# Performance work log

Hardware: AMD Instinct MI355X
Metric: run time of the kernel (lower is better)

The kernel has to match this reference:

```python
import jax, jax.numpy as jnp
import numpy as np

B, S, D, H, DFF = 4, 2048, 1024, 16, 4096
HD = D // H
EPS = 1e-12

def _layernorm(x, g, b):
    mu = jnp.mean(x, axis=-1, keepdims=True)
    var = jnp.mean(jnp.square(x - mu), axis=-1, keepdims=True)
    return (x - mu) * jax.lax.rsqrt(var + EPS) * g + b

def setup_inputs() -> dict:
    key = jax.random.key(0)
    ks = jax.random.split(key, 12)
    sd = 0.02
    inp = {
        'hidden_states': jax.random.normal(ks[0], (B, S, D), jnp.float32),
        'attention_mask': jnp.zeros((B, 1, 1, S), jnp.float32),
        'Wq': jax.random.normal(ks[1], (D, D), jnp.float32) * sd,
        'bq': jnp.zeros((D,), jnp.float32),
        'Wk': jax.random.normal(ks[2], (D, D), jnp.float32) * sd,
        'bk': jnp.zeros((D,), jnp.float32),
        'Wv': jax.random.normal(ks[3], (D, D), jnp.float32) * sd,
        'bv': jnp.zeros((D,), jnp.float32),
        'Wo': jax.random.normal(ks[4], (D, D), jnp.float32) * sd,
        'bo': jnp.zeros((D,), jnp.float32),
        'ln1_g': jnp.ones((D,), jnp.float32),
        'ln1_b': jnp.zeros((D,), jnp.float32),
        'Wi': jax.random.normal(ks[5], (D, DFF), jnp.float32) * sd,
        'bi': jnp.zeros((DFF,), jnp.float32),
        'Wo2': jax.random.normal(ks[6], (DFF, D), jnp.float32) * sd,
        'bo2': jnp.zeros((D,), jnp.float32),
        'ln2_g': jnp.ones((D,), jnp.float32),
        'ln2_b': jnp.zeros((D,), jnp.float32),
    }
    return inp

def reference(hidden_states, attention_mask, Wq, bq, Wk, bk, Wv, bv, Wo, bo,
              ln1_g, ln1_b, Wi, bi, Wo2, bo2, ln2_g, ln2_b):
    x = hidden_states  # [B,S,D]
    # project and split heads -> [B,H,S,hd]
    def heads(t):
        return t.reshape(B, S, H, HD).transpose(0, 2, 1, 3)
    q = heads(x @ Wq + bq)
    k = heads(x @ Wk + bk)
    v = heads(x @ Wv + bv)
    scores = jnp.einsum('bhqd,bhkd->bhqk', q, k) / np.float32(np.sqrt(HD))
    scores = scores + attention_mask  # additive mask broadcast [B,1,1,S]
    weights = jax.nn.softmax(scores, axis=-1)
    ctx = jnp.einsum('bhqk,bhkd->bhqd', weights, v)
    ctx = ctx.transpose(0, 2, 1, 3).reshape(B, S, D)
    attn_out = _layernorm(ctx @ Wo + bo + x, ln1_g, ln1_b)
    # FFN (gelu) with residual + LayerNorm
    h = jax.nn.gelu(attn_out @ Wi + bi, approximate=False)
    out = _layernorm(h @ Wo2 + bo2 + attn_out, ln2_g, ln2_b)
    return out
```

## Files before the change

### kernel.cpp

```cpp
#include <hip/hip_runtime.h>
#include <hip/hip_bf16.h>
#include <math.h>

#define B_   4
#define S_   2048
#define D_   1024
#define H_   16
#define HD_  64
#define DFF_ 4096
#define M_   (B_*S_)

typedef __bf16 bf16x8 __attribute__((ext_vector_type(8)));
typedef __bf16 bf16x4 __attribute__((ext_vector_type(4)));
typedef float  floatx4 __attribute__((ext_vector_type(4)));

__device__ __forceinline__ float  b2f(__bf16 v) { return (float)v; }
__device__ __forceinline__ __bf16 f2b(float v)  { return (__bf16)v; }

__device__ __forceinline__ void async_ld16(const void* g, void* l) {
    __builtin_amdgcn_global_load_lds(
        (const __attribute__((address_space(1))) unsigned int*)g,
        (__attribute__((address_space(3))) unsigned int*)l, 16, 0, 0);
}

__global__ void transpose_conv_kernel(const float* __restrict__ in,
                                      __bf16* __restrict__ out, int R, int C,
                                      float scale)
{
    __shared__ float t[32][33];
    int c0 = blockIdx.x * 32, r0 = blockIdx.y * 32;
    int tx = threadIdx.x, ty = threadIdx.y;
    for (int i = ty; i < 32; i += 8)
        t[i][tx] = in[(long)(r0 + i) * C + c0 + tx];
    __syncthreads();
    for (int i = ty; i < 32; i += 8)
        out[(long)(c0 + i) * R + r0 + tx] = f2b(t[tx][i] * scale);
}

__global__ void vt_transpose_kernel(const __bf16* __restrict__ qkv,
                                    __bf16* __restrict__ vtg)
{
    __shared__ __bf16 t[32][34];
    int b  = blockIdx.z;
    int h  = blockIdx.y >> 1;
    int d0 = (blockIdx.y & 1) * 32;
    int s0 = blockIdx.x * 32;
    int tx = threadIdx.x, ty = threadIdx.y;
    for (int i = ty; i < 32; i += 8)
        t[i][tx] = qkv[(long)(b * S_ + s0 + i) * 3072 + 2048 + h * 64 + d0 + tx];
    __syncthreads();
    for (int i = ty; i < 32; i += 8)
        vtg[((long)(b * H_ + h) * 64 + d0 + i) * S_ + s0 + tx] = t[tx][i];
}

__global__ void f2b_kernel(const float* __restrict__ in, __bf16* __restrict__ out,
                           long n)
{
    long i = ((long)blockIdx.x * 256 + threadIdx.x) * 8;
    if (i >= n) return;
    float4 a = *(const float4*)&in[i];
    float4 c = *(const float4*)&in[i + 4];
    union { __bf16 h[8]; uint4 u; } p;
    p.h[0] = f2b(a.x); p.h[1] = f2b(a.y); p.h[2] = f2b(a.z); p.h[3] = f2b(a.w);
    p.h[4] = f2b(c.x); p.h[5] = f2b(c.y); p.h[6] = f2b(c.z); p.h[7] = f2b(c.w);
    *(uint4*)&out[i] = p.u;
}

__global__ void bias_concat_kernel(const float* __restrict__ bq,
                                   const float* __restrict__ bk,
                                   const float* __restrict__ bv,
                                   float* __restrict__ dst)
{
    int i = blockIdx.x * 256 + threadIdx.x;
    if (i >= 3 * D_) return;
    float v = (i < D_) ? bq[i] * 0.125f
            : (i < 2 * D_) ? bk[i - D_] : bv[i - 2 * D_];
    dst[i] = v;
}

template<int MODE>
__global__ __launch_bounds__(256, 2)
void gemm_kernel(const __bf16* __restrict__ A, const __bf16* __restrict__ Bt,
                 const float* __restrict__ bias, const float* __restrict__ resid,
                 float* __restrict__ Cf, __bf16* __restrict__ Cb,
                 int M, int N, int K)
{
    __shared__ __bf16 sA[128 * 64];
    __shared__ __bf16 sB[128 * 64];

    const int tid  = threadIdx.x;
    const int lane = tid & 63;
    const int wave = tid >> 6;
    const int wm   = (wave >> 1) * 64;
    const int wn   = (wave & 1) * 64;
    const long bm  = (long)blockIdx.y * 128;
    const long bn  = (long)blockIdx.x * 128;

    floatx4 acc[4][4];
#pragma unroll
    for (int i = 0; i < 4; ++i)
#pragma unroll
        for (int j = 0; j < 4; ++j)
#pragma unroll
            for (int r = 0; r < 4; ++r) acc[i][j][r] = 0.0f;

    const int mrow = lane & 15;
    const int quad = lane >> 4;
    const int koff0 = ((0 * 4 + quad) ^ (mrow & 7)) * 8;
    const int koff1 = ((1 * 4 + quad) ^ (mrow & 7)) * 8;

    for (int k0 = 0; k0 < K; k0 += 64) {
        __syncthreads();
#pragma unroll
        for (int t = 0; t < 4; ++t) {
            int ci  = tid + t * 256;
            int row = ci >> 3;
            int col = ((ci & 7) ^ (row & 7)) << 3;
            async_ld16(A  + (bm + row) * (long)K + k0 + col, &sA[ci * 8]);
            async_ld16(Bt + (bn + row) * (long)K + k0 + col, &sB[ci * 8]);
        }
        __syncthreads();

#pragma unroll
        for (int s = 0; s < 2; ++s) {
            const int ko = s ? koff1 : koff0;
            bf16x8 a[4], b[4];
#pragma unroll
            for (int i = 0; i < 4; ++i)
                a[i] = *(const bf16x8*)&sA[(wm + i * 16 + mrow) * 64 + ko];
#pragma unroll
            for (int j = 0; j < 4; ++j)
                b[j] = *(const bf16x8*)&sB[(wn + j * 16 + mrow) * 64 + ko];
#pragma unroll
            for (int i = 0; i < 4; ++i)
#pragma unroll
                for (int j = 0; j < 4; ++j)
                    acc[i][j] = __builtin_amdgcn_mfma_f32_16x16x32_bf16(
                        a[i], b[j], acc[i][j], 0, 0, 0);
        }
    }

    const int rq = quad * 4;
    const int cn = lane & 15;
#pragma unroll
    for (int i = 0; i < 4; ++i) {
#pragma unroll
        for (int j = 0; j < 4; ++j) {
            long col = bn + wn + j * 16 + cn;
            float bv = bias[col];
#pragma unroll
            for (int r = 0; r < 4; ++r) {
                long row = bm + wm + i * 16 + rq + r;
                float v = acc[i][j][r] + bv;
                if (MODE == 0) {
                    Cb[row * N + col] = f2b(v);
                } else if (MODE == 1) {
                    Cf[row * N + col] = v + resid[row * N + col];
                } else {
                    float g = 0.5f * v * (1.0f + erff(v * 0.70710678118654752f));
                    Cb[row * N + col] = f2b(g);
                }
            }
        }
    }
}

__global__ __launch_bounds__(256, 2)
void attn_kernel(const __bf16* __restrict__ QKV, const __bf16* __restrict__ VT,
                 const float* __restrict__ mask, __bf16* __restrict__ ctx)
{
    __shared__ __bf16 Ks[2][64 * 64];
    __shared__ __bf16 Vt[2][64 * 64];
    __shared__ __bf16 Ps[64 * 64];

    const int tid  = threadIdx.x;
    const int lane = tid & 63;
    const int wave = tid >> 6;
    const int w16  = wave * 16;
    const int b    = blockIdx.z, h = blockIdx.y;
    const int q0   = blockIdx.x * 64;
    const int cn   = lane & 15;
    const int quad = lane >> 4;
    const int rq   = quad * 4;
    const int koff0 = ((0 * 4 + quad) ^ (cn & 7)) * 8;
    const int koff1 = ((1 * 4 + quad) ^ (cn & 7)) * 8;

    const long vbase = ((long)(b * H_ + h) * 64) * S_;

    auto STAGE = [&](int bufi, int k0) {
#pragma unroll
        for (int t = 0; t < 2; ++t) {
            int ci = tid + t * 256;
            int r  = ci >> 3;
            int cz = ((ci & 7) ^ (r & 7)) << 3;
            async_ld16(QKV + (long)(b * S_ + k0 + r) * 3072 + 1024 + h * 64 + cz,
                       &Ks[bufi][ci * 8]);
            async_ld16(VT + vbase + (long)r * S_ + k0 + cz, &Vt[bufi][ci * 8]);
        }
    };

#pragma unroll
    for (int t = 0; t < 2; ++t) {
        int ci = tid + t * 256;
        int qr = ci >> 3, dc = ((ci & 7) ^ (qr & 7)) << 3;
        async_ld16(QKV + (long)(b * S_ + q0 + qr) * 3072 + h * 64 + dc,
                   &Ps[ci * 8]);
    }
    STAGE(0, 0);
    asm volatile("s_waitcnt vmcnt(0)" ::: "memory");
    __builtin_amdgcn_s_barrier();
    __builtin_amdgcn_sched_barrier(0);

    const bf16x8 aq0 = *(const bf16x8*)&Ps[(w16 + cn) * 64 + koff0];
    const bf16x8 aq1 = *(const bf16x8*)&Ps[(w16 + cn) * 64 + koff1];

    float l_[4];
    floatx4 o_[4];
#pragma unroll
    for (int r = 0; r < 4; ++r) l_[r] = 0.0f;
#pragma unroll
    for (int jt = 0; jt < 4; ++jt)
#pragma unroll
        for (int r = 0; r < 4; ++r) o_[jt][r] = 0.0f;

    int cur = 0;
    for (int k0 = 0; k0 < S_; k0 += 64) {
        if (k0 + 64 < S_) STAGE(cur ^ 1, k0 + 64);

        floatx4 st[4];
#pragma unroll
        for (int jt = 0; jt < 4; ++jt)
#pragma unroll
            for (int r = 0; r < 4; ++r) st[jt][r] = 0.0f;
#pragma unroll
        for (int jt = 0; jt < 4; ++jt) {
            bf16x8 b0 = *(const bf16x8*)&Ks[cur][(jt * 16 + cn) * 64 + koff0];
            bf16x8 b1 = *(const bf16x8*)&Ks[cur][(jt * 16 + cn) * 64 + koff1];
            st[jt] = __builtin_amdgcn_mfma_f32_16x16x32_bf16(aq0, b0, st[jt], 0, 0, 0);
            st[jt] = __builtin_amdgcn_mfma_f32_16x16x32_bf16(aq1, b1, st[jt], 0, 0, 0);
        }
#pragma unroll
        for (int jt = 0; jt < 4; ++jt) {
            float mv = mask[(long)b * S_ + k0 + jt * 16 + cn] - 8.0f;
#pragma unroll
            for (int r = 0; r < 4; ++r) {
                float p = __expf(st[jt][r] + mv);
                st[jt][r] = p;
                l_[r] += p;
            }
        }
#pragma unroll
        for (int jt = 0; jt < 4; ++jt)
#pragma unroll
            for (int r = 0; r < 4; ++r) {
                int prow = w16 + rq + r;
                int pcol = (((jt * 2 + (cn >> 3)) ^ (prow & 7)) << 3) + (cn & 7);
                Ps[prow * 64 + pcol] = f2b(st[jt][r]);
            }

        {
            bf16x8 ap0 = *(const bf16x8*)&Ps[(w16 + cn) * 64 + koff0];
            bf16x8 ap1 = *(const bf16x8*)&Ps[(w16 + cn) * 64 + koff1];
#pragma unroll
            for (int jt = 0; jt < 4; ++jt) {
                bf16x8 b0 = *(const bf16x8*)&Vt[cur][(jt * 16 + cn) * 64 + koff0];
                bf16x8 b1 = *(const bf16x8*)&Vt[cur][(jt * 16 + cn) * 64 + koff1];
                o_[jt] = __builtin_amdgcn_mfma_f32_16x16x32_bf16(ap0, b0, o_[jt], 0, 0, 0);
                o_[jt] = __builtin_amdgcn_mfma_f32_16x16x32_bf16(ap1, b1, o_[jt], 0, 0, 0);
            }
        }

        asm volatile("s_waitcnt vmcnt(0) lgkmcnt(0)" ::: "memory");
        __builtin_amdgcn_s_barrier();
        __builtin_amdgcn_sched_barrier(0);
        cur ^= 1;
    }

#pragma unroll
    for (int r = 0; r < 4; ++r) {
        float l = l_[r];
        l += __shfl_xor(l, 1);
        l += __shfl_xor(l, 2);
        l += __shfl_xor(l, 4);
        l += __shfl_xor(l, 8);
        float linv = 1.0f / l;
        long rowg = (long)(b * S_ + q0 + w16 + rq + r) * D_ + h * 64;
#pragma unroll
        for (int jt = 0; jt < 4; ++jt)
            ctx[rowg + jt * 16 + cn] = f2b(o_[jt][r] * linv);
    }
}

__global__ __launch_bounds__(256)
void ln_kernel(const float* __restrict__ X, const float* __restrict__ gamma,
               const float* __restrict__ beta, float* __restrict__ out,
               __bf16* __restrict__ outb)
{
    const long row = blockIdx.x;
    const int tid = threadIdx.x;
    const float* x = X + row * D_;
    float4 v = *(const float4*)&x[tid * 4];
    float s  = v.x + v.y + v.z + v.w;
    float s2 = v.x * v.x + v.y * v.y + v.z * v.z + v.w * v.w;
    for (int off = 32; off > 0; off >>= 1) {
        s  += __shfl_down(s, off);
        s2 += __shfl_down(s2, off);
    }
    __shared__ float red[8];
    int wave = tid >> 6, lane = tid & 63;
    if (lane == 0) { red[wave] = s; red[4 + wave] = s2; }
    __syncthreads();
    float ts  = red[0] + red[1] + red[2] + red[3];
    float ts2 = red[4] + red[5] + red[6] + red[7];
    float mu  = ts * (1.0f / D_);
    float var = ts2 * (1.0f / D_) - mu * mu;
    float rs  = rsqrtf(fmaxf(var, 0.0f) + 1e-12f);
    float4 g = *(const float4*)&gamma[tid * 4];
    float4 b = *(const float4*)&beta[tid * 4];
    float4 o;
    o.x = (v.x - mu) * rs * g.x + b.x;
    o.y = (v.y - mu) * rs * g.y + b.y;
    o.z = (v.z - mu) * rs * g.z + b.z;
    o.w = (v.w - mu) * rs * g.w + b.w;
    *(float4*)&out[row * D_ + tid * 4] = o;
    if (outb) {
        bf16x4 ob;
        ob[0] = f2b(o.x); ob[1] = f2b(o.y); ob[2] = f2b(o.z); ob[3] = f2b(o.w);
        *(bf16x4*)&outb[row * D_ + tid * 4] = ob;
    }
}

extern "C" void kernel_launch(void* const* d_in, const int* in_sizes, int n_in,
                              void* d_out, int out_size, void* d_ws, size_t ws_size,
                              hipStream_t stream)
{
    const float* hid  = (const float*)d_in[0];
    const float* mask = (const float*)d_in[1];
    const float* Wq   = (const float*)d_in[2];
    const float* bq   = (const float*)d_in[3];
    const float* Wk   = (const float*)d_in[4];
    const float* bk   = (const float*)d_in[5];
    const float* Wv   = (const float*)d_in[6];
    const float* bv   = (const float*)d_in[7];
    const float* Wo   = (const float*)d_in[8];
    const float* bo   = (const float*)d_in[9];
    const float* g1   = (const float*)d_in[10];
    const float* b1   = (const float*)d_in[11];
    const float* Wi   = (const float*)d_in[12];
    const float* bi   = (const float*)d_in[13];
    const float* Wo2  = (const float*)d_in[14];
    const float* bo2  = (const float*)d_in[15];
    const float* g2   = (const float*)d_in[16];
    const float* b2   = (const float*)d_in[17];
    float* out = (float*)d_out;

    char* w = (char*)d_ws;
    auto take = [&](size_t bytes) { char* p = w; w += bytes; return p; };
    __bf16* wqkvb = (__bf16*)take((size_t)3 * D_ * D_ * 2);
    __bf16* wob   = (__bf16*)take((size_t)D_ * D_ * 2);
    __bf16* wib   = (__bf16*)take((size_t)D_ * DFF_ * 2);
    __bf16* wo2b  = (__bf16*)take((size_t)D_ * DFF_ * 2);
    float*  qkvbias = (float*)take(16384);
    __bf16* qkv   = (__bf16*)take((size_t)M_ * 3 * D_ * 2);
    __bf16* ctxb  = (__bf16*)take((size_t)M_ * D_ * 2);
    __bf16* hb    = (__bf16*)take((size_t)M_ * D_ * 2);
    float*  tmp      = (float*)take((size_t)M_ * D_ * 4);
    float*  attn_out = (float*)take((size_t)M_ * D_ * 4);
    __bf16* hbuf = qkv;
    __bf16* vtg  = hb;
    __bf16* attn_out_b = hb;
    (void)in_sizes; (void)n_in; (void)out_size; (void)ws_size;

    dim3 tb(32, 8);
    transpose_conv_kernel<<<dim3(D_/32, D_/32), tb, 0, stream>>>(Wq, wqkvb,            D_, D_, 0.125f);
    transpose_conv_kernel<<<dim3(D_/32, D_/32), tb, 0, stream>>>(Wk, wqkvb + D_*D_,    D_, D_, 1.0f);
    transpose_conv_kernel<<<dim3(D_/32, D_/32), tb, 0, stream>>>(Wv, wqkvb + 2*D_*D_,  D_, D_, 1.0f);
    transpose_conv_kernel<<<dim3(D_/32, D_/32), tb, 0, stream>>>(Wo, wob, D_, D_, 1.0f);
    transpose_conv_kernel<<<dim3(DFF_/32, D_/32), tb, 0, stream>>>(Wi, wib, D_, DFF_, 1.0f);
    transpose_conv_kernel<<<dim3(D_/32, DFF_/32), tb, 0, stream>>>(Wo2, wo2b, DFF_, D_, 1.0f);
    bias_concat_kernel<<<12, 256, 0, stream>>>(bq, bk, bv, qkvbias);
    f2b_kernel<<<(M_*D_/8 + 255)/256, 256, 0, stream>>>(hid, hb, (long)M_*D_);

    gemm_kernel<0><<<dim3(3*D_/128, M_/128), 256, 0, stream>>>(
        hb, wqkvb, qkvbias, nullptr, nullptr, qkv, M_, 3*D_, D_);

    vt_transpose_kernel<<<dim3(S_/32, H_*2, B_), tb, 0, stream>>>(qkv, vtg);

    attn_kernel<<<dim3(S_/64, H_, B_), 256, 0, stream>>>(qkv, vtg, mask, ctxb);

    gemm_kernel<1><<<dim3(D_/128, M_/128), 256, 0, stream>>>(
        ctxb, wob, bo, hid, tmp, nullptr, M_, D_, D_);
    ln_kernel<<<M_, 256, 0, stream>>>(tmp, g1, b1, attn_out, attn_out_b);

    gemm_kernel<2><<<dim3(DFF_/128, M_/128), 256, 0, stream>>>(
        attn_out_b, wib, bi, nullptr, nullptr, hbuf, M_, DFF_, D_);
    gemm_kernel<1><<<dim3(D_/128, M_/128), 256, 0, stream>>>(
        hbuf, wo2b, bo2, attn_out, tmp, nullptr, M_, D_, DFF_);
    ln_kernel<<<M_, 256, 0, stream>>>(tmp, g2, b2, out, nullptr);
}
```

Before: 569.0 us.

## Fuse prep kernels into one launch, remap attention blocks per XCD, prefetch mask

Merges the six weight transpose-convert launches, the bias concat and the hidden-state bf16 conversion into a single prep kernel dispatched on block index, removing seven launches. The attention grid becomes one-dimensional and is remapped so blocks of the same (batch, head) land on the same XCD, which should improve L2 reuse of K/V. Mask values are now prefetched one tile ahead, and MFMA sections are wrapped in s_setprio to favour matrix issue. The branchy prep kernel adds divergence-free but uneven block work.

```diff
diff --git a/kernel.cpp b/kernel.cpp
--- a/kernel.cpp
+++ b/kernel.cpp
@@ -23,18 +23,51 @@
         (__attribute__((address_space(3))) unsigned int*)l, 16, 0, 0);
 }
 
-__global__ void transpose_conv_kernel(const float* __restrict__ in,
-                                      __bf16* __restrict__ out, int R, int C,
-                                      float scale)
+__global__ __launch_bounds__(256)
+void prep_kernel(const float* __restrict__ Wq, const float* __restrict__ Wk,
+                 const float* __restrict__ Wv, const float* __restrict__ Wo,
+                 const float* __restrict__ Wi, const float* __restrict__ Wo2,
+                 const float* __restrict__ bq, const float* __restrict__ bk,
+                 const float* __restrict__ bv, const float* __restrict__ hid,
+                 __bf16* __restrict__ wqkvb, __bf16* __restrict__ wob,
+                 __bf16* __restrict__ wib, __bf16* __restrict__ wo2b,
+                 float* __restrict__ qkvbias, __bf16* __restrict__ hb)
 {
     __shared__ float t[32][33];
-    int c0 = blockIdx.x * 32, r0 = blockIdx.y * 32;
-    int tx = threadIdx.x, ty = threadIdx.y;
-    for (int i = ty; i < 32; i += 8)
-        t[i][tx] = in[(long)(r0 + i) * C + c0 + tx];
-    __syncthreads();
-    for (int i = ty; i < 32; i += 8)
-        out[(long)(c0 + i) * R + r0 + tx] = f2b(t[tx][i] * scale);
+    const int bid = blockIdx.x;
+    const int tid = threadIdx.x;
+
+    if (bid < 12288) {
+        const float* in; __bf16* outp; int R, C, nx, lid; float scale = 1.0f;
+        if (bid < 1024)      { in = Wq;  outp = wqkvb;           R = D_;   C = D_;   nx = 32;  lid = bid;        scale = 0.125f; }
+        else if (bid < 2048) { in = Wk;  outp = wqkvb + D_*D_;   R = D_;   C = D_;   nx = 32;  lid = bid - 1024; }
+        else if (bid < 3072) { in = Wv;  outp = wqkvb + 2*D_*D_; R = D_;   C = D_;   nx = 32;  lid = bid - 2048; }
+        else if (bid < 4096) { in = Wo;  outp = wob;             R = D_;   C = D_;   nx = 32;  lid = bid - 3072; }
+        else if (bid < 8192) { in = Wi;  outp = wib;             R = D_;   C = DFF_; nx = 128; lid = bid - 4096; }
+        else                 { in = Wo2; outp = wo2b;            R = DFF_; C = D_;   nx = 32;  lid = bid - 8192; }
+        const int c0 = (lid % nx) * 32, r0 = (lid / nx) * 32;
+        const int tx = tid & 31, ty = tid >> 5;
+        for (int i = ty; i < 32; i += 8)
+            t[i][tx] = in[(long)(r0 + i) * C + c0 + tx];
+        __syncthreads();
+        for (int i = ty; i < 32; i += 8)
+            outp[(long)(c0 + i) * R + r0 + tx] = f2b(t[tx][i] * scale);
+    } else if (bid < 16384) {
+        long i = ((long)(bid - 12288) * 256 + tid) * 8;
+        if (i >= (long)M_ * D_) return;
+        float4 a = *(const float4*)&hid[i];
+        float4 c = *(const float4*)&hid[i + 4];
+        union { __bf16 h[8]; uint4 u; } p;
+        p.h[0] = f2b(a.x); p.h[1] = f2b(a.y); p.h[2] = f2b(a.z); p.h[3] = f2b(a.w);
+        p.h[4] = f2b(c.x); p.h[5] = f2b(c.y); p.h[6] = f2b(c.z); p.h[7] = f2b(c.w);
+        *(uint4*)&hb[i] = p.u;
+    } else {
+        int i = (bid - 16384) * 256 + tid;
+        if (i >= 3 * D_) return;
+        float v = (i < D_) ? bq[i] * 0.125f
+                : (i < 2 * D_) ? bk[i - D_] : bv[i - 2 * D_];
+        qkvbias[i] = v;
+    }
 }
 
 __global__ void vt_transpose_kernel(const __bf16* __restrict__ qkv,
@@ -51,31 +84,6 @@
     __syncthreads();
     for (int i = ty; i < 32; i += 8)
         vtg[((long)(b * H_ + h) * 64 + d0 + i) * S_ + s0 + tx] = t[tx][i];
-}
-
-__global__ void f2b_kernel(const float* __restrict__ in, __bf16* __restrict__ out,
-                           long n)
-{
-    long i = ((long)blockIdx.x * 256 + threadIdx.x) * 8;
-    if (i >= n) return;
-    float4 a = *(const float4*)&in[i];
-    float4 c = *(const float4*)&in[i + 4];
-    union { __bf16 h[8]; uint4 u; } p;
-    p.h[0] = f2b(a.x); p.h[1] = f2b(a.y); p.h[2] = f2b(a.z); p.h[3] = f2b(a.w);
-    p.h[4] = f2b(c.x); p.h[5] = f2b(c.y); p.h[6] = f2b(c.z); p.h[7] = f2b(c.w);
-    *(uint4*)&out[i] = p.u;
-}
-
-__global__ void bias_concat_kernel(const float* __restrict__ bq,
-                                   const float* __restrict__ bk,
-                                   const float* __restrict__ bv,
-                                   float* __restrict__ dst)
-{
-    int i = blockIdx.x * 256 + threadIdx.x;
-    if (i >= 3 * D_) return;
-    float v = (i < D_) ? bq[i] * 0.125f
-            : (i < 2 * D_) ? bk[i - D_] : bv[i - 2 * D_];
-    dst[i] = v;
 }
 
 template<int MODE>
@@ -177,8 +185,15 @@
     const int lane = tid & 63;
     const int wave = tid >> 6;
     const int w16  = wave * 16;
-    const int b    = blockIdx.z, h = blockIdx.y;
-    const int q0   = blockIdx.x * 64;
+
+    const int ibk  = blockIdx.x;
+    const int xcd  = ibk & 7;
+    const int tt   = ibk >> 3;
+    const int head_lin = xcd * 8 + (tt >> 5);
+    const int q0   = (tt & 31) * 64;
+    const int b    = head_lin >> 4;
+    const int h    = head_lin & 15;
+
     const int cn   = lane & 15;
     const int quad = lane >> 4;
     const int rq   = quad * 4;
@@ -207,6 +222,10 @@
                    &Ps[ci * 8]);
     }
     STAGE(0, 0);
+    float mv[4];
+#pragma unroll
+    for (int jt = 0; jt < 4; ++jt)
+        mv[jt] = mask[(long)b * S_ + jt * 16 + cn] - 8.0f;
     asm volatile("s_waitcnt vmcnt(0)" ::: "memory");
     __builtin_amdgcn_s_barrier();
     __builtin_amdgcn_sched_barrier(0);
@@ -225,13 +244,20 @@
 
     int cur = 0;
     for (int k0 = 0; k0 < S_; k0 += 64) {
-        if (k0 + 64 < S_) STAGE(cur ^ 1, k0 + 64);
+        float mvn[4];
+        if (k0 + 64 < S_) {
+            STAGE(cur ^ 1, k0 + 64);
+#pragma unroll
+            for (int jt = 0; jt < 4; ++jt)
+                mvn[jt] = mask[(long)b * S_ + k0 + 64 + jt * 16 + cn] - 8.0f;
+        }
 
         floatx4 st[4];
 #pragma unroll
         for (int jt = 0; jt < 4; ++jt)
 #pragma unroll
             for (int r = 0; r < 4; ++r) st[jt][r] = 0.0f;
+        __builtin_amdgcn_s_setprio(1);
 #pragma unroll
         for (int jt = 0; jt < 4; ++jt) {
             bf16x8 b0 = *(const bf16x8*)&Ks[cur][(jt * 16 + cn) * 64 + koff0];
@@ -239,12 +265,12 @@
             st[jt] = __builtin_amdgcn_mfma_f32_16x16x32_bf16(aq0, b0, st[jt], 0, 0, 0);
             st[jt] = __builtin_amdgcn_mfma_f32_16x16x32_bf16(aq1, b1, st[jt], 0, 0, 0);
         }
+        __builtin_amdgcn_s_setprio(0);
 #pragma unroll
         for (int jt = 0; jt < 4; ++jt) {
-            float mv = mask[(long)b * S_ + k0 + jt * 16 + cn] - 8.0f;
 #pragma unroll
             for (int r = 0; r < 4; ++r) {
-                float p = __expf(st[jt][r] + mv);
+                float p = __expf(st[jt][r] + mv[jt]);
                 st[jt][r] = p;
                 l_[r] += p;
             }
@@ -261,6 +287,7 @@
         {
             bf16x8 ap0 = *(const bf16x8*)&Ps[(w16 + cn) * 64 + koff0];
             bf16x8 ap1 = *(const bf16x8*)&Ps[(w16 + cn) * 64 + koff1];
+            __builtin_amdgcn_s_setprio(1);
 #pragma unroll
             for (int jt = 0; jt < 4; ++jt) {
                 bf16x8 b0 = *(const bf16x8*)&Vt[cur][(jt * 16 + cn) * 64 + koff0];
@@ -268,11 +295,16 @@
                 o_[jt] = __builtin_amdgcn_mfma_f32_16x16x32_bf16(ap0, b0, o_[jt], 0, 0, 0);
                 o_[jt] = __builtin_amdgcn_mfma_f32_16x16x32_bf16(ap1, b1, o_[jt], 0, 0, 0);
             }
+            __builtin_amdgcn_s_setprio(0);
         }
 
         asm volatile("s_waitcnt vmcnt(0) lgkmcnt(0)" ::: "memory");
         __builtin_amdgcn_s_barrier();
         __builtin_amdgcn_sched_barrier(0);
+        if (k0 + 64 < S_) {
+#pragma unroll
+            for (int jt = 0; jt < 4; ++jt) mv[jt] = mvn[jt];
+        }
         cur ^= 1;
     }
 
@@ -371,22 +403,17 @@
     __bf16* attn_out_b = hb;
     (void)in_sizes; (void)n_in; (void)out_size; (void)ws_size;
 
-    dim3 tb(32, 8);
-    transpose_conv_kernel<<<dim3(D_/32, D_/32), tb, 0, stream>>>(Wq, wqkvb,            D_, D_, 0.125f);
-    transpose_conv_kernel<<<dim3(D_/32, D_/32), tb, 0, stream>>>(Wk, wqkvb + D_*D_,    D_, D_, 1.0f);
-    transpose_conv_kernel<<<dim3(D_/32, D_/32), tb, 0, stream>>>(Wv, wqkvb + 2*D_*D_,  D_, D_, 1.0f);
-    transpose_conv_kernel<<<dim3(D_/32, D_/32), tb, 0, stream>>>(Wo, wob, D_, D_, 1.0f);
-    transpose_conv_kernel<<<dim3(DFF_/32, D_/32), tb, 0, stream>>>(Wi, wib, D_, DFF_, 1.0f);
-    transpose_conv_kernel<<<dim3(D_/32, DFF_/32), tb, 0, stream>>>(Wo2, wo2b, DFF_, D_, 1.0f);
-    bias_concat_kernel<<<12, 256, 0, stream>>>(bq, bk, bv, qkvbias);
-    f2b_kernel<<<(M_*D_/8 + 255)/256, 256, 0, stream>>>(hid, hb, (long)M_*D_);
+    prep_kernel<<<16396, 256, 0, stream>>>(
+        Wq, Wk, Wv, Wo, Wi, Wo2, bq, bk, bv, hid,
+        wqkvb, wob, wib, wo2b, qkvbias, hb);
 
     gemm_kernel<0><<<dim3(3*D_/128, M_/128), 256, 0, stream>>>(
         hb, wqkvb, qkvbias, nullptr, nullptr, qkv, M_, 3*D_, D_);
 
+    dim3 tb(32, 8);
     vt_transpose_kernel<<<dim3(S_/32, H_*2, B_), tb, 0, stream>>>(qkv, vtg);
 
-    attn_kernel<<<dim3(S_/64, H_, B_), 256, 0, stream>>>(qkv, vtg, mask, ctxb);
+    attn_kernel<<<2048, 256, 0, stream>>>(qkv, vtg, mask, ctxb);
 
     gemm_kernel<1><<<dim3(D_/128, M_/128), 256, 0, stream>>>(
         ctxb, wob, bo, hid, tmp, nullptr, M_, D_, D_);
```

Measured after the change: 547.4 us. 1.04x faster.
